# Performance work log

Hardware: AMD Instinct MI355X
Metric: run time of the kernel (lower is better)

The kernel has to match this reference:

```python
import jax, jax.numpy as jnp
import numpy as np
import math

N = 65536
C_IN = 64
C_OUT = 64
NS = 16
BN_EPS = 1e-5


def _knn_idx(p_np, k):
    # exact kNN (including self), chunked to bound memory
    p_np = np.asarray(p_np, np.float32)
    n = p_np.shape[0]
    sq = (p_np * p_np).sum(1)
    idx = np.empty((n, k), np.int32)
    cs = 1024
    for s in range(0, n, cs):
        q = p_np[s:s + cs]
        d = sq[None, :] - 2.0 * (q @ p_np.T) + (q * q).sum(1)[:, None]
        part = np.argpartition(d, k, axis=1)[:, :k]
        dd = np.take_along_axis(d, part, 1)
        order = np.argsort(dd, axis=1)
        idx[s:s + cs] = np.take_along_axis(part, order, 1).astype(np.int32)
    return idx


def setup_inputs() -> dict:
    key = jax.random.key(0)
    ks = jax.random.split(key, 12)
    p = jax.random.uniform(ks[0], (N, 3), dtype=jnp.float32) * 10.0
    x = jax.random.normal(ks[1], (N, C_IN), dtype=jnp.float32)
    idx = jnp.asarray(_knn_idx(np.asarray(p), NS))  # (N, NS) int32
    s_in = 1.0 / math.sqrt(C_IN)
    Wq = jax.random.normal(ks[2], (C_IN, C_OUT), dtype=jnp.float32) * s_in
    bq = jnp.zeros((C_OUT,), jnp.float32)
    Wk = jax.random.normal(ks[3], (C_IN, C_OUT), dtype=jnp.float32) * s_in
    bk = jnp.zeros((C_OUT,), jnp.float32)
    Wv = jax.random.normal(ks[4], (C_IN, C_OUT), dtype=jnp.float32) * s_in
    bv = jnp.zeros((C_OUT,), jnp.float32)
    Wp1 = jax.random.normal(ks[5], (3, 3), dtype=jnp.float32) * (1.0 / math.sqrt(3))
    bp1 = jnp.zeros((3,), jnp.float32)
    gamma = jnp.ones((3,), jnp.float32)
    beta = jnp.zeros((3,), jnp.float32)
    Wp2 = jax.random.normal(ks[6], (3, C_OUT), dtype=jnp.float32) * (1.0 / math.sqrt(3))
    bp2 = jnp.zeros((C_OUT,), jnp.float32)
    return {"p": p, "x": x, "idx": idx, "Wq": Wq, "bq": bq, "Wk": Wk, "bk": bk,
            "Wv": Wv, "bv": bv, "Wp1": Wp1, "bp1": bp1, "gamma": gamma,
            "beta": beta, "Wp2": Wp2, "bp2": bp2}


def reference(p, x, idx, Wq, bq, Wk, bk, Wv, bv, Wp1, bp1, gamma, beta, Wp2, bp2):
    x_q = x @ Wq + bq                       # (N, Co)
    x_k = (x @ Wk + bk)[idx]                # gather: (N, NS, Co)
    x_v = (x @ Wv + bv)[idx]                # gather: (N, NS, Co)
    p_r = p[idx] - p[:, None, :]            # relative coords (N, NS, 3)
    # linear_p: Linear(3,3) -> BatchNorm1d(3) (training stats) -> ReLU -> Linear(3,Co)
    h = p_r @ Wp1 + bp1                     # (N, NS, 3)
    mean = h.mean(axis=(0, 1))
    var = ((h - mean) ** 2).mean(axis=(0, 1))
    h = (h - mean) * jax.lax.rsqrt(var + BN_EPS) * gamma + beta
    h = jax.nn.relu(h)
    p_emb = h @ Wp2 + bp2                   # (N, NS, Co)
    x_k = x_k + p_emb
    x_v = x_v + p_emb
    attn = (x_q[:, None, :] * x_k).sum(-1) / math.sqrt(C_OUT)  # (N, NS)
    w = jax.nn.softmax(attn, axis=1)
    return (x_v * w[:, :, None]).sum(axis=1)  # (N, Co)
```

## Files before the change

kernel.cpp:

```cpp
#include <hip/hip_runtime.h>

#define N_PTS 65536
#define NSS 16
#define C 64

typedef __attribute__((ext_vector_type(8))) short short8;
typedef __attribute__((ext_vector_type(4))) float f32x4;

__device__ __forceinline__ unsigned short f2bf(float v) {
  unsigned int u = __float_as_uint(v);
  u += 0x7fffu + ((u >> 16) & 1u);
  return (unsigned short)(u >> 16);
}
__device__ __forceinline__ float bflo(unsigned int u) { return __uint_as_float(u << 16); }
__device__ __forceinline__ float bfhi(unsigned int u) { return __uint_as_float(u & 0xffff0000u); }

__global__ void init_kernel(const float* __restrict__ Wq, const float* __restrict__ Wk,
                            const float* __restrict__ Wv, float* __restrict__ stats,
                            unsigned short* __restrict__ wt) {
  const int t = blockIdx.x * 256 + threadIdx.x;
  if (t < 9) stats[t] = 0.f;
  if (t < 192 * 64) {
    const int k = t / 192, ng = t % 192;
    const int mat = ng >> 6, n = ng & 63;
    const float* W = mat == 0 ? Wq : (mat == 1 ? Wk : Wv);
    wt[ng * 64 + k] = f2bf(W[k * 64 + n]);
  }
}

__global__ __launch_bounds__(256) void qkv_kernel(
    const float* __restrict__ x, const unsigned short* __restrict__ wt,
    const float* __restrict__ bq, const float* __restrict__ bk, const float* __restrict__ bv,
    const float* __restrict__ p, const int* __restrict__ idx,
    float* __restrict__ xq, unsigned short* __restrict__ kv, float* __restrict__ stats) {
  __shared__ unsigned short xs[64][72];
  const int t = threadIdx.x;
  const int p0 = blockIdx.x * 64;
  const float4* x4 = (const float4*)x;
#pragma unroll
  for (int j = 0; j < 4; ++j) {
    const int id = j * 256 + t;
    const int row = id >> 4, cg = id & 15;
    const float4 v = x4[(p0 + row) * 16 + cg];
    ushort4 h4;
    h4.x = f2bf(v.x); h4.y = f2bf(v.y); h4.z = f2bf(v.z); h4.w = f2bf(v.w);
    *(ushort4*)&xs[row][cg * 4] = h4;
  }
  __syncthreads();

  const int lane = t & 63, wave = t >> 6;
  const int quad = lane >> 4, lr = lane & 15;
  const int mrow = wave * 16 + lr;
  const short8 a0 = *(const short8*)&xs[mrow][quad * 8];
  const short8 a1 = *(const short8*)&xs[mrow][quad * 8 + 32];
#pragma unroll
  for (int nt = 0; nt < 12; ++nt) {
    const unsigned short* bpr = wt + (nt * 16 + lr) * 64 + quad * 8;
    const short8 b0 = *(const short8*)bpr;
    const short8 b1 = *(const short8*)(bpr + 32);
    f32x4 acc = {0.f, 0.f, 0.f, 0.f};
    acc = __builtin_amdgcn_mfma_f32_16x16x32_bf16(a0, b0, acc, 0, 0, 0);
    acc = __builtin_amdgcn_mfma_f32_16x16x32_bf16(a1, b1, acc, 0, 0, 0);
    const int mat = nt >> 2;
    const int c = (nt & 3) * 16 + lr;
    const float bias = (mat == 0 ? bq : (mat == 1 ? bk : bv))[c];
#pragma unroll
    for (int r = 0; r < 4; ++r) {
      const int pt = p0 + wave * 16 + quad * 4 + r;
      const float val = acc[r] + bias;
      if (mat == 0) xq[pt * 64 + c] = val;
      else kv[pt * 128 + (mat == 2 ? 64 : 0) + c] = f2bf(val);
    }
  }

  const int tid = blockIdx.x * 256 + t;
  float s0 = 0, s1 = 0, s2 = 0, s00 = 0, s01 = 0, s02 = 0, s11 = 0, s12 = 0, s22 = 0;
  for (int s = tid; s < N_PTS * NSS; s += 262144) {
    const int n = s >> 4;
    const int j = idx[s];
    const float dx = p[j * 3 + 0] - p[n * 3 + 0];
    const float dy = p[j * 3 + 1] - p[n * 3 + 1];
    const float dz = p[j * 3 + 2] - p[n * 3 + 2];
    s0 += dx; s1 += dy; s2 += dz;
    s00 += dx * dx; s01 += dx * dy; s02 += dx * dz;
    s11 += dy * dy; s12 += dy * dz; s22 += dz * dz;
  }
#pragma unroll
  for (int m = 1; m < 64; m <<= 1) {
    s0 += __shfl_xor(s0, m, 64);  s1 += __shfl_xor(s1, m, 64);  s2 += __shfl_xor(s2, m, 64);
    s00 += __shfl_xor(s00, m, 64); s01 += __shfl_xor(s01, m, 64); s02 += __shfl_xor(s02, m, 64);
    s11 += __shfl_xor(s11, m, 64); s12 += __shfl_xor(s12, m, 64); s22 += __shfl_xor(s22, m, 64);
  }
  __shared__ float part[4][9];
  if (lane == 0) {
    part[wave][0] = s0;  part[wave][1] = s1;  part[wave][2] = s2;
    part[wave][3] = s00; part[wave][4] = s01; part[wave][5] = s02;
    part[wave][6] = s11; part[wave][7] = s12; part[wave][8] = s22;
  }
  __syncthreads();
  if (t < 9) {
    atomicAdd(&stats[t], part[0][t] + part[1][t] + part[2][t] + part[3][t]);
  }
}

__device__ __forceinline__ float merge2(float a, float b, int bit, int lane) {
  const bool hi = (lane & bit) != 0;
  const float keep = hi ? b : a;
  const float send = hi ? a : b;
  return keep + __shfl_xor(send, bit, 64);
}
template <int CTRL>
__device__ __forceinline__ float dppmv(float x) {
  return __int_as_float(__builtin_amdgcn_update_dpp(
      __float_as_int(x), __float_as_int(x), CTRL, 0xF, 0xF, true));
}
__device__ __forceinline__ float red16_add(float x) {
  x += dppmv<0xB1>(x);
  x += dppmv<0x4E>(x);
  x += __shfl_xor(x, 4, 64);
  x += __shfl_xor(x, 8, 64);
  return x;
}
__device__ __forceinline__ float red16_max(float x) {
  x = fmaxf(x, dppmv<0xB1>(x));
  x = fmaxf(x, dppmv<0x4E>(x));
  x = fmaxf(x, __shfl_xor(x, 4, 64));
  x = fmaxf(x, __shfl_xor(x, 8, 64));
  return x;
}
__device__ __forceinline__ float red8_add(float x) {
  x += dppmv<0xB1>(x);
  x += dppmv<0x4E>(x);
  x += __shfl_xor(x, 4, 64);
  return x;
}
__device__ __forceinline__ float dot8q(const float4 a, const float4 b, const uint4 r) {
  float s = a.x * bflo(r.x);
  s = fmaf(a.y, bfhi(r.x), s);
  s = fmaf(a.z, bflo(r.y), s);
  s = fmaf(a.w, bfhi(r.y), s);
  s = fmaf(b.x, bflo(r.z), s);
  s = fmaf(b.y, bfhi(r.z), s);
  s = fmaf(b.z, bflo(r.w), s);
  s = fmaf(b.w, bfhi(r.w), s);
  return s;
}
__device__ __forceinline__ float dot8f(const float4 a, const float4 b,
                                       const float4 c, const float4 d) {
  float s = a.x * c.x;
  s = fmaf(a.y, c.y, s); s = fmaf(a.z, c.z, s); s = fmaf(a.w, c.w, s);
  s = fmaf(b.x, d.x, s); s = fmaf(b.y, d.y, s); s = fmaf(b.z, d.z, s); s = fmaf(b.w, d.w, s);
  return s;
}

__global__ __launch_bounds__(256, 4) void attn_kernel(
    const float* __restrict__ p, const int* __restrict__ idx,
    const float* __restrict__ xq, const unsigned short* __restrict__ kv,
    const float* __restrict__ stats,
    const float* __restrict__ Wp1, const float* __restrict__ bp1,
    const float* __restrict__ gamma, const float* __restrict__ beta,
    const float* __restrict__ Wp2, const float* __restrict__ bp2,
    float* __restrict__ out) {
  const int lane = threadIdx.x & 63;
  const int n = (blockIdx.x * blockDim.x + threadIdx.x) >> 6;
  const int slice = lane >> 3;
  const int rlo = lane & 7;

  const int jall = idx[n * NSS + (lane & 15)];
  const int jb0 = __shfl(jall, rlo, 64);
  const int jb1 = __shfl(jall, rlo | 8, 64);

  const uint4 kr0 = *(const uint4*)(kv + (size_t)jb0 * 128 + slice * 8);
  const uint4 kr1 = *(const uint4*)(kv + (size_t)jb1 * 128 + slice * 8);
  const uint4 vr0 = *(const uint4*)(kv + (size_t)jb0 * 128 + 64 + slice * 8);
  const uint4 vr1 = *(const uint4*)(kv + (size_t)jb1 * 128 + 64 + slice * 8);
  const float pjx = p[jall * 3 + 0], pjy = p[jall * 3 + 1], pjz = p[jall * 3 + 2];
  const float pnx = p[n * 3 + 0], pny = p[n * 3 + 1], pnz = p[n * 3 + 2];

  const float4* xq4 = (const float4*)xq;
  const float4 qa = xq4[n * 16 + slice * 2], qb = xq4[n * 16 + slice * 2 + 1];
  const float4* w24 = (const float4*)Wp2;
  const float4 w20a = w24[slice * 2],      w20b = w24[slice * 2 + 1];
  const float4 w21a = w24[16 + slice * 2], w21b = w24[16 + slice * 2 + 1];
  const float4 w22a = w24[32 + slice * 2], w22b = w24[32 + slice * 2 + 1];
  const float4* bp24 = (const float4*)bp2;
  const float4 b2a = bp24[slice * 2], b2b = bp24[slice * 2 + 1];

  const float invM = 1.0f / (float)(N_PTS * NSS);
  const float m0 = stats[0] * invM, m1 = stats[1] * invM, m2 = stats[2] * invM;
  const float cv00 = stats[3] * invM - m0 * m0, cv01 = stats[4] * invM - m0 * m1;
  const float cv02 = stats[5] * invM - m0 * m2, cv11 = stats[6] * invM - m1 * m1;
  const float cv12 = stats[7] * invM - m1 * m2, cv22 = stats[8] * invM - m2 * m2;
  float e[12];
#pragma unroll
  for (int tt = 0; tt < 3; ++tt) {
    const float w0 = Wp1[0 * 3 + tt], w1 = Wp1[1 * 3 + tt], w2 = Wp1[2 * 3 + tt];
    const float mh = w0 * m0 + w1 * m1 + w2 * m2 + bp1[tt];
    const float var = w0 * w0 * cv00 + w1 * w1 * cv11 + w2 * w2 * cv22 +
                      2.f * (w0 * w1 * cv01 + w0 * w2 * cv02 + w1 * w2 * cv12);
    const float sc = gamma[tt] * rsqrtf(var + 1e-5f);
    e[tt] = w0 * sc; e[3 + tt] = w1 * sc; e[6 + tt] = w2 * sc;
    e[9 + tt] = (bp1[tt] - mh) * sc + beta[tt];
  }

  float S = merge2(dot8q(qa, qb, kr0), dot8q(qa, qb, kr1), 8, lane);
  S += __shfl_xor(S, 16, 64);
  S += __shfl_xor(S, 32, 64);

  const float tp0 = dot8f(qa, qb, w20a, w20b);
  const float tp1 = dot8f(qa, qb, w21a, w21b);
  const float tp2 = dot8f(qa, qb, w22a, w22b);
  const float tp3 = dot8f(qa, qb, b2a, b2b);
  float T = merge2(merge2(tp0, tp1, 8, lane), merge2(tp2, tp3, 8, lane), 16, lane);
  T += __shfl_xor(T, 32, 64);
  const float t0 = __shfl(T, 0, 64), t1 = __shfl(T, 8, 64);
  const float t2 = __shfl(T, 16, 64), t3 = __shfl(T, 24, 64);

  const float dx = pjx - pnx, dy = pjy - pny, dz = pjz - pnz;
  const float h0 = fmaxf(fmaf(dx, e[0], fmaf(dy, e[3], fmaf(dz, e[6], e[9]))), 0.f);
  const float h1 = fmaxf(fmaf(dx, e[1], fmaf(dy, e[4], fmaf(dz, e[7], e[10]))), 0.f);
  const float h2 = fmaxf(fmaf(dx, e[2], fmaf(dy, e[5], fmaf(dz, e[8], e[11]))), 0.f);

  const float a = (S + fmaf(h0, t0, fmaf(h1, t1, fmaf(h2, t2, t3)))) * 0.125f;
  const float mx = red16_max(a);
  const float ex = __expf(a - mx);
  const float den = red16_add(ex);
  const float w = ex / den;

  const float H0 = red16_add(w * h0);
  const float H1 = red16_add(w * h1);
  const float H2 = red16_add(w * h2);

  const float wb0 = __shfl(w, rlo, 64);
  const float wb1 = __shfl(w, rlo | 8, 64);
  const unsigned int v0c[4] = {vr0.x, vr0.y, vr0.z, vr0.w};
  const unsigned int v1c[4] = {vr1.x, vr1.y, vr1.z, vr1.w};
  float o[8];
#pragma unroll
  for (int q2 = 0; q2 < 4; ++q2) {
    o[2 * q2]     = fmaf(wb0, bflo(v0c[q2]), wb1 * bflo(v1c[q2]));
    o[2 * q2 + 1] = fmaf(wb0, bfhi(v0c[q2]), wb1 * bfhi(v1c[q2]));
  }
#pragma unroll
  for (int j = 0; j < 8; ++j) o[j] = red8_add(o[j]);

  const float w20f[8] = {w20a.x, w20a.y, w20a.z, w20a.w, w20b.x, w20b.y, w20b.z, w20b.w};
  const float w21f[8] = {w21a.x, w21a.y, w21a.z, w21a.w, w21b.x, w21b.y, w21b.z, w21b.w};
  const float w22f[8] = {w22a.x, w22a.y, w22a.z, w22a.w, w22b.x, w22b.y, w22b.z, w22b.w};
  const float b2f[8]  = {b2a.x, b2a.y, b2a.z, b2a.w, b2b.x, b2b.y, b2b.z, b2b.w};
#pragma unroll
  for (int j = 0; j < 8; ++j)
    o[j] += fmaf(H0, w20f[j], fmaf(H1, w21f[j], fmaf(H2, w22f[j], b2f[j])));

  if (rlo == 0) {
    float4 oa = {o[0], o[1], o[2], o[3]};
    float4 ob = {o[4], o[5], o[6], o[7]};
    float4* o4 = (float4*)out;
    o4[n * 16 + slice * 2] = oa;
    o4[n * 16 + slice * 2 + 1] = ob;
  }
}

extern "C" void kernel_launch(void* const* d_in, const int* in_sizes, int n_in,
                              void* d_out, int out_size, void* d_ws, size_t ws_size,
                              hipStream_t stream) {
  const float* p     = (const float*)d_in[0];
  const float* x     = (const float*)d_in[1];
  const int*   idx   = (const int*)d_in[2];
  const float* Wq    = (const float*)d_in[3];
  const float* bq    = (const float*)d_in[4];
  const float* Wk    = (const float*)d_in[5];
  const float* bk    = (const float*)d_in[6];
  const float* Wv    = (const float*)d_in[7];
  const float* bv    = (const float*)d_in[8];
  const float* Wp1   = (const float*)d_in[9];
  const float* bp1   = (const float*)d_in[10];
  const float* gamma = (const float*)d_in[11];
  const float* beta  = (const float*)d_in[12];
  const float* Wp2   = (const float*)d_in[13];
  const float* bp2   = (const float*)d_in[14];
  float* out = (float*)d_out;

  float* stats = (float*)d_ws;
  unsigned short* wt = (unsigned short*)((char*)d_ws + 256);
  float* xq = (float*)((char*)d_ws + 32768);
  unsigned short* kv = (unsigned short*)((char*)d_ws + 32768 + (size_t)N_PTS * C * 4);

  init_kernel<<<48, 256, 0, stream>>>(Wq, Wk, Wv, stats, wt);
  qkv_kernel<<<N_PTS / 64, 256, 0, stream>>>(x, wt, bq, bk, bv, p, idx, xq, kv, stats);
  attn_kernel<<<N_PTS / 4, 256, 0, stream>>>(p, idx, xq, kv, stats, Wp1, bp1, gamma, beta,
                                             Wp2, bp2, out);
}
```

Measured before the change: 183.4 us.

## Morton-sort query order, store bf16 q, use MFMA for attention scores

Each run builds a spatial Morton-cell counting sort of the points (histogram, scan, scatter) so the attention kernel visits queries in a cache-friendly order. It also stores q as bf16 next to k/v in a single 192-wide row and precomputes q·Wp2 and q·bp2 per point in the QKV kernel through a folded weight matrix. The attention kernel then computes the q·k scores with MFMA instead of shuffle reductions. The cost is three extra small kernel launches plus a memset, atomics, and lower precision for q.

```diff
diff --git a/kernel.cpp b/kernel.cpp
--- a/kernel.cpp
+++ b/kernel.cpp
@@ -15,9 +15,24 @@
 __device__ __forceinline__ float bflo(unsigned int u) { return __uint_as_float(u << 16); }
 __device__ __forceinline__ float bfhi(unsigned int u) { return __uint_as_float(u & 0xffff0000u); }
 
-__global__ void init_kernel(const float* __restrict__ Wq, const float* __restrict__ Wk,
-                            const float* __restrict__ Wv, float* __restrict__ stats,
-                            unsigned short* __restrict__ wt) {
+__device__ __forceinline__ int cell_of(float px, float py, float pz) {
+  const int cx = min(15, max(0, (int)(px * 1.6f)));
+  const int cy = min(15, max(0, (int)(py * 1.6f)));
+  const int cz = min(15, max(0, (int)(pz * 1.6f)));
+  int m = 0;
+#pragma unroll
+  for (int b = 0; b < 4; ++b)
+    m |= (((cx >> b) & 1) << (3 * b + 2)) | (((cy >> b) & 1) << (3 * b + 1)) |
+         (((cz >> b) & 1) << (3 * b));
+  return m;
+}
+
+__global__ __launch_bounds__(256) void init_kernel(
+    const float* __restrict__ Wq, const float* __restrict__ Wk, const float* __restrict__ Wv,
+    const float* __restrict__ Wp2, const float* __restrict__ bp2, const float* __restrict__ bq,
+    const float* __restrict__ p,
+    float* __restrict__ stats, unsigned short* __restrict__ wt,
+    unsigned short* __restrict__ wtq, float* __restrict__ tb, int* __restrict__ hist) {
   const int t = blockIdx.x * 256 + threadIdx.x;
   if (t < 9) stats[t] = 0.f;
   if (t < 192 * 64) {
@@ -26,14 +41,62 @@
     const float* W = mat == 0 ? Wq : (mat == 1 ? Wk : Wv);
     wt[ng * 64 + k] = f2bf(W[k * 64 + n]);
   }
+  if (t < 1024) {
+    const int row = t >> 6, k = t & 63;
+    float val = 0.f;
+    if (row < 4) {
+      const float* B2 = (row == 3) ? bp2 : (Wp2 + row * 64);
+      for (int c2 = 0; c2 < 64; ++c2) val += Wq[k * 64 + c2] * B2[c2];
+    }
+    wtq[t] = f2bf(val);
+  }
+  if (t >= 1024 && t < 1028) {
+    const int n2 = t - 1024;
+    const float* B2 = (n2 == 3) ? bp2 : (Wp2 + n2 * 64);
+    float val = 0.f;
+    for (int c2 = 0; c2 < 64; ++c2) val += bq[c2] * B2[c2];
+    tb[n2] = val;
+  }
+  if (t < N_PTS) {
+    atomicAdd(&hist[cell_of(p[t * 3 + 0], p[t * 3 + 1], p[t * 3 + 2])], 1);
+  }
+}
+
+__global__ __launch_bounds__(256) void scan_kernel(const int* __restrict__ hist,
+                                                   int* __restrict__ offs) {
+  __shared__ int part[256];
+  const int t = threadIdx.x;
+  int sum = 0;
+#pragma unroll
+  for (int i = 0; i < 16; ++i) sum += hist[t * 16 + i];
+  part[t] = sum;
+  __syncthreads();
+  if (t == 0) {
+    int run = 0;
+    for (int i = 0; i < 256; ++i) { const int v = part[i]; part[i] = run; run += v; }
+  }
+  __syncthreads();
+  int run = part[t];
+  for (int i = 0; i < 16; ++i) { offs[t * 16 + i] = run; run += hist[t * 16 + i]; }
+}
+
+__global__ __launch_bounds__(256) void scatter_kernel(const float* __restrict__ p,
+                                                      int* __restrict__ offs,
+                                                      int* __restrict__ perm) {
+  const int t = blockIdx.x * 256 + threadIdx.x;
+  const int cidx = cell_of(p[t * 3 + 0], p[t * 3 + 1], p[t * 3 + 2]);
+  const int pos = atomicAdd(&offs[cidx], 1);
+  perm[pos] = t;
 }
 
 __global__ __launch_bounds__(256) void qkv_kernel(
     const float* __restrict__ x, const unsigned short* __restrict__ wt,
+    const unsigned short* __restrict__ wtq, const float* __restrict__ tb,
     const float* __restrict__ bq, const float* __restrict__ bk, const float* __restrict__ bv,
     const float* __restrict__ p, const int* __restrict__ idx,
-    float* __restrict__ xq, unsigned short* __restrict__ kv, float* __restrict__ stats) {
-  __shared__ unsigned short xs[64][72];
+    unsigned short* __restrict__ kvq, float* __restrict__ tq, float* __restrict__ stats) {
+  __shared__ __align__(16) unsigned short xs[64][72];
+  __shared__ __align__(16) unsigned short kvs[64][192];
   const int t = threadIdx.x;
   const int p0 = blockIdx.x * 64;
   const float4* x4 = (const float4*)x;
@@ -66,12 +129,31 @@
     const float bias = (mat == 0 ? bq : (mat == 1 ? bk : bv))[c];
 #pragma unroll
     for (int r = 0; r < 4; ++r) {
-      const int pt = p0 + wave * 16 + quad * 4 + r;
-      const float val = acc[r] + bias;
-      if (mat == 0) xq[pt * 64 + c] = val;
-      else kv[pt * 128 + (mat == 2 ? 64 : 0) + c] = f2bf(val);
+      const int row = wave * 16 + quad * 4 + r;
+      kvs[row][mat * 64 + c] = f2bf(acc[r] + bias);
     }
   }
+  {
+    const unsigned short* bpr = wtq + lr * 64 + quad * 8;
+    const short8 b0 = *(const short8*)bpr;
+    const short8 b1 = *(const short8*)(bpr + 32);
+    f32x4 acc = {0.f, 0.f, 0.f, 0.f};
+    acc = __builtin_amdgcn_mfma_f32_16x16x32_bf16(a0, b0, acc, 0, 0, 0);
+    acc = __builtin_amdgcn_mfma_f32_16x16x32_bf16(a1, b1, acc, 0, 0, 0);
+    if (lr < 4) {
+      const float tbv = tb[lr];
+#pragma unroll
+      for (int r = 0; r < 4; ++r) {
+        const int pt = p0 + wave * 16 + quad * 4 + r;
+        tq[pt * 4 + lr] = acc[r] + tbv;
+      }
+    }
+  }
+  __syncthreads();
+  const uint4* kvs4 = (const uint4*)&kvs[0][0];
+  uint4* dst = (uint4*)(kvq + (size_t)p0 * 192);
+#pragma unroll
+  for (int j = 0; j < 6; ++j) dst[j * 256 + t] = kvs4[j * 256 + t];
 
   const int tid = blockIdx.x * 256 + t;
   float s0 = 0, s1 = 0, s2 = 0, s00 = 0, s01 = 0, s02 = 0, s11 = 0, s12 = 0, s22 = 0;
@@ -103,12 +185,6 @@
   }
 }
 
-__device__ __forceinline__ float merge2(float a, float b, int bit, int lane) {
-  const bool hi = (lane & bit) != 0;
-  const float keep = hi ? b : a;
-  const float send = hi ? a : b;
-  return keep + __shfl_xor(send, bit, 64);
-}
 template <int CTRL>
 __device__ __forceinline__ float dppmv(float x) {
   return __int_as_float(__builtin_amdgcn_update_dpp(
@@ -134,51 +210,36 @@
   x += __shfl_xor(x, 4, 64);
   return x;
 }
-__device__ __forceinline__ float dot8q(const float4 a, const float4 b, const uint4 r) {
-  float s = a.x * bflo(r.x);
-  s = fmaf(a.y, bfhi(r.x), s);
-  s = fmaf(a.z, bflo(r.y), s);
-  s = fmaf(a.w, bfhi(r.y), s);
-  s = fmaf(b.x, bflo(r.z), s);
-  s = fmaf(b.y, bfhi(r.z), s);
-  s = fmaf(b.z, bflo(r.w), s);
-  s = fmaf(b.w, bfhi(r.w), s);
-  return s;
-}
-__device__ __forceinline__ float dot8f(const float4 a, const float4 b,
-                                       const float4 c, const float4 d) {
-  float s = a.x * c.x;
-  s = fmaf(a.y, c.y, s); s = fmaf(a.z, c.z, s); s = fmaf(a.w, c.w, s);
-  s = fmaf(b.x, d.x, s); s = fmaf(b.y, d.y, s); s = fmaf(b.z, d.z, s); s = fmaf(b.w, d.w, s);
-  return s;
-}
 
 __global__ __launch_bounds__(256, 4) void attn_kernel(
     const float* __restrict__ p, const int* __restrict__ idx,
-    const float* __restrict__ xq, const unsigned short* __restrict__ kv,
-    const float* __restrict__ stats,
+    const unsigned short* __restrict__ kvq, const float* __restrict__ tq,
+    const int* __restrict__ perm, const float* __restrict__ stats,
     const float* __restrict__ Wp1, const float* __restrict__ bp1,
     const float* __restrict__ gamma, const float* __restrict__ beta,
     const float* __restrict__ Wp2, const float* __restrict__ bp2,
     float* __restrict__ out) {
   const int lane = threadIdx.x & 63;
-  const int n = (blockIdx.x * blockDim.x + threadIdx.x) >> 6;
-  const int slice = lane >> 3;
-  const int rlo = lane & 7;
-
-  const int jall = idx[n * NSS + (lane & 15)];
+  const int wave = threadIdx.x >> 6;
+  const int b = blockIdx.x;
+  const int sb = (b & 7) * (N_PTS / 4 / 8) + (b >> 3);
+  const int n = perm[sb * 4 + wave];
+  const int quad = lane >> 4, s = lane & 15;
+  const int slice = lane >> 3, rlo = lane & 7;
+
+  const int jall = idx[n * NSS + s];
+  const short8 a0 = *(const short8*)(kvq + (size_t)n * 192 + quad * 8);
+  const short8 a1 = *(const short8*)(kvq + (size_t)n * 192 + quad * 8 + 32);
+  const short8 bk0 = *(const short8*)(kvq + (size_t)jall * 192 + 64 + quad * 8);
+  const short8 bk1 = *(const short8*)(kvq + (size_t)jall * 192 + 64 + quad * 8 + 32);
   const int jb0 = __shfl(jall, rlo, 64);
   const int jb1 = __shfl(jall, rlo | 8, 64);
-
-  const uint4 kr0 = *(const uint4*)(kv + (size_t)jb0 * 128 + slice * 8);
-  const uint4 kr1 = *(const uint4*)(kv + (size_t)jb1 * 128 + slice * 8);
-  const uint4 vr0 = *(const uint4*)(kv + (size_t)jb0 * 128 + 64 + slice * 8);
-  const uint4 vr1 = *(const uint4*)(kv + (size_t)jb1 * 128 + 64 + slice * 8);
+  const uint4 vr0 = *(const uint4*)(kvq + (size_t)jb0 * 192 + 128 + slice * 8);
+  const uint4 vr1 = *(const uint4*)(kvq + (size_t)jb1 * 192 + 128 + slice * 8);
+  const float4 t4 = ((const float4*)tq)[n];
   const float pjx = p[jall * 3 + 0], pjy = p[jall * 3 + 1], pjz = p[jall * 3 + 2];
   const float pnx = p[n * 3 + 0], pny = p[n * 3 + 1], pnz = p[n * 3 + 2];
 
-  const float4* xq4 = (const float4*)xq;
-  const float4 qa = xq4[n * 16 + slice * 2], qb = xq4[n * 16 + slice * 2 + 1];
   const float4* w24 = (const float4*)Wp2;
   const float4 w20a = w24[slice * 2],      w20b = w24[slice * 2 + 1];
   const float4 w21a = w24[16 + slice * 2], w21b = w24[16 + slice * 2 + 1];
@@ -203,25 +264,17 @@
     e[9 + tt] = (bp1[tt] - mh) * sc + beta[tt];
   }
 
-  float S = merge2(dot8q(qa, qb, kr0), dot8q(qa, qb, kr1), 8, lane);
-  S += __shfl_xor(S, 16, 64);
-  S += __shfl_xor(S, 32, 64);
-
-  const float tp0 = dot8f(qa, qb, w20a, w20b);
-  const float tp1 = dot8f(qa, qb, w21a, w21b);
-  const float tp2 = dot8f(qa, qb, w22a, w22b);
-  const float tp3 = dot8f(qa, qb, b2a, b2b);
-  float T = merge2(merge2(tp0, tp1, 8, lane), merge2(tp2, tp3, 8, lane), 16, lane);
-  T += __shfl_xor(T, 32, 64);
-  const float t0 = __shfl(T, 0, 64), t1 = __shfl(T, 8, 64);
-  const float t2 = __shfl(T, 16, 64), t3 = __shfl(T, 24, 64);
+  f32x4 acc = {0.f, 0.f, 0.f, 0.f};
+  acc = __builtin_amdgcn_mfma_f32_16x16x32_bf16(a0, bk0, acc, 0, 0, 0);
+  acc = __builtin_amdgcn_mfma_f32_16x16x32_bf16(a1, bk1, acc, 0, 0, 0);
+  const float S = acc[0];
 
   const float dx = pjx - pnx, dy = pjy - pny, dz = pjz - pnz;
   const float h0 = fmaxf(fmaf(dx, e[0], fmaf(dy, e[3], fmaf(dz, e[6], e[9]))), 0.f);
   const float h1 = fmaxf(fmaf(dx, e[1], fmaf(dy, e[4], fmaf(dz, e[7], e[10]))), 0.f);
   const float h2 = fmaxf(fmaf(dx, e[2], fmaf(dy, e[5], fmaf(dz, e[8], e[11]))), 0.f);
 
-  const float a = (S + fmaf(h0, t0, fmaf(h1, t1, fmaf(h2, t2, t3)))) * 0.125f;
+  const float a = (S + fmaf(h0, t4.x, fmaf(h1, t4.y, fmaf(h2, t4.z, t4.w)))) * 0.125f;
   const float mx = red16_max(a);
   const float ex = __expf(a - mx);
   const float den = red16_add(ex);
@@ -281,13 +334,22 @@
   const float* bp2   = (const float*)d_in[14];
   float* out = (float*)d_out;
 
-  float* stats = (float*)d_ws;
-  unsigned short* wt = (unsigned short*)((char*)d_ws + 256);
-  float* xq = (float*)((char*)d_ws + 32768);
-  unsigned short* kv = (unsigned short*)((char*)d_ws + 32768 + (size_t)N_PTS * C * 4);
-
-  init_kernel<<<48, 256, 0, stream>>>(Wq, Wk, Wv, stats, wt);
-  qkv_kernel<<<N_PTS / 64, 256, 0, stream>>>(x, wt, bq, bk, bv, p, idx, xq, kv, stats);
-  attn_kernel<<<N_PTS / 4, 256, 0, stream>>>(p, idx, xq, kv, stats, Wp1, bp1, gamma, beta,
-                                             Wp2, bp2, out);
-}
+  char* w = (char*)d_ws;
+  float* stats        = (float*)w;
+  float* tb           = (float*)(w + 64);
+  unsigned short* wt  = (unsigned short*)(w + 256);
+  unsigned short* wtq = (unsigned short*)(w + 25088);
+  int* hist           = (int*)(w + 32768);
+  int* offs           = (int*)(w + 49152);
+  int* perm           = (int*)(w + 65536);
+  unsigned short* kvq = (unsigned short*)(w + 327680);
+  float* tq           = (float*)(w + 25493504);
+
+  hipMemsetAsync(hist, 0, 4096 * sizeof(int), stream);
+  init_kernel<<<256, 256, 0, stream>>>(Wq, Wk, Wv, Wp2, bp2, bq, p, stats, wt, wtq, tb, hist);
+  scan_kernel<<<1, 256, 0, stream>>>(hist, offs);
+  scatter_kernel<<<256, 256, 0, stream>>>(p, offs, perm);
+  qkv_kernel<<<N_PTS / 64, 256, 0, stream>>>(x, wt, wtq, tb, bq, bk, bv, p, idx, kvq, tq, stats);
+  attn_kernel<<<N_PTS / 4, 256, 0, stream>>>(p, idx, kvq, tq, perm, stats, Wp1, bp1, gamma,
+                                             beta, Wp2, bp2, out);
+}
```

New measurement: 208.2 us. 13.5% more time.
